# Kernel optimization log

Measured on AMD Instinct MI355X. Metric: run time of the kernel, lower is better.

Reference implementation:

```python
import jax, jax.numpy as jnp
import numpy as np

N, D_IN, D_OUT = 4096, 1024, 1024

def setup_inputs() -> dict:
    key = jax.random.key(0)
    k1, k2, k3, k4 = jax.random.split(key, 4)
    x = jax.random.normal(k1, (N, D_IN), dtype=jnp.float32)
    # original uses torch.rand (uniform [0,1)) for params
    w_query = jax.random.uniform(k2, (D_IN, D_OUT), dtype=jnp.float32)
    w_key = jax.random.uniform(k3, (D_IN, D_OUT), dtype=jnp.float32)
    w_value = jax.random.uniform(k4, (D_IN, D_OUT), dtype=jnp.float32)
    return {"x": x, "w_query": w_query, "w_key": w_key, "w_value": w_value}

def reference(x, w_query, w_key, w_value):
    queries = x @ w_query          # [N, d_out]
    keys = x @ w_key               # [N, d_out]
    values = x @ w_value           # [N, d_out]
    scale = keys.shape[-1] ** 0.5
    scores = queries @ keys.T      # [N, N]
    attn = jax.nn.softmax(scores / scale, axis=-1)
    return attn @ values           # [N, d_out]
```

## Files before the change

kernel.cpp:

```cpp
#include <hip/hip_runtime.h>
#include <math.h>

#define NROWS 4096
#define DDIM  1024

typedef __attribute__((ext_vector_type(8))) short short8;
typedef __attribute__((ext_vector_type(4))) float f32x4;

__device__ __forceinline__ ushort f2bf(float v) {
  union { float f; uint32_t u; } c; c.f = v;
  uint32_t u = c.u;
  uint32_t lsb = (u >> 16) & 1u;
  u += 0x7fffu + lsb;
  return (ushort)(u >> 16);
}
__device__ __forceinline__ float bf2f(ushort h) {
  union { uint32_t u; float f; } c; c.u = ((uint32_t)h) << 16;
  return c.f;
}

__device__ __forceinline__ size_t pidx(int r, int c, int ldt) {
  return ((size_t)((r >> 4) * ldt + (c >> 5))) * 512 +
         ((c >> 3) & 3) * 128 + (r & 15) * 8 + (c & 7);
}
__device__ __forceinline__ size_t pidxs(int r, int c, int ldt) {
  return ((size_t)((r >> 4) * ldt + (c >> 5))) * 1024 +
         ((c >> 3) & 3) * 128 + (r & 15) * 8 + (c & 7);
}

__global__ __launch_bounds__(256) void prep(const float* __restrict__ x,
                                            const float* __restrict__ wq,
                                            const float* __restrict__ wk,
                                            const float* __restrict__ wv,
                                            ushort* Xc,
                                            ushort* Wqc, ushort* Wkc, ushort* Wvh) {
  __shared__ float tl[32][33];
  const int b = blockIdx.x, t = threadIdx.x;
  if (b < 1024) {
    const float4* src = (const float4*)x;
#pragma unroll
    for (int r = 0; r < 4; ++r) {
      int i = b * 1024 + r * 256 + t;
      int row = i >> 8;
      int c = (i & 255) << 2;
      float4 v = src[i];
      ushort4 h, l;
      h.x = f2bf(v.x); l.x = f2bf(v.x - bf2f(h.x));
      h.y = f2bf(v.y); l.y = f2bf(v.y - bf2f(h.y));
      h.z = f2bf(v.z); l.z = f2bf(v.z - bf2f(h.z));
      h.w = f2bf(v.w); l.w = f2bf(v.w - bf2f(h.w));
      size_t o = pidxs(row, c, DDIM / 32);
      *(ushort4*)(Xc + o) = h;
      *(ushort4*)(Xc + o + 512) = l;
    }
  } else {
    const int z = (b - 1024) >> 10;
    const int tile = (b - 1024) & 1023;
    const float* src = z == 0 ? wq : (z == 1 ? wk : wv);
    const int r0 = (tile >> 5) * 32;
    const int c0 = (tile & 31) * 32;
    const int tx = t & 31, ty = t >> 5;
    for (int i = ty; i < 32; i += 8)
      tl[i][tx] = src[(size_t)(r0 + i) * DDIM + c0 + tx];
    __syncthreads();
    if (z == 2) {
      for (int i = ty; i < 32; i += 8) {
        float v = tl[tx][i];
        Wvh[pidx(c0 + i, r0 + tx, DDIM / 32)] = f2bf(v);
      }
    } else {
      ushort* d = z == 0 ? Wqc : Wkc;
      for (int i = ty; i < 32; i += 8) {
        float v = tl[tx][i];
        ushort h = f2bf(v);
        size_t o = pidxs(c0 + i, r0 + tx, DDIM / 32);
        d[o] = h;
        d[o + 512] = f2bf(v - bf2f(h));
      }
    }
  }
}

template <int MI, bool SPLIT, int KT, int SA, int SB>
__device__ __forceinline__ void direct_gemm(const ushort* __restrict__ A,
                                            const ushort* __restrict__ B,
                                            int m0, int n0, f32x4 (*acc)[4]) {
  const int t = threadIdx.x;
  const int wv = t >> 6, ln = t & 63;
  const int arb = (wv >> 1) * (MI * 16), crb = (wv & 1) * 64;
  const int ra = (m0 + arb) >> 4;
  const int rb = (n0 + crb) >> 4;

  uint oA[MI], oB[4];
#pragma unroll
  for (int i = 0; i < MI; ++i) oA[i] = (uint)(ra + i) * (uint)(KT * SA) + (uint)ln * 8u;
#pragma unroll
  for (int j = 0; j < 4; ++j) oB[j] = (uint)(rb + j) * (uint)(KT * SB) + (uint)ln * 8u;

  short8 ah0[MI], al0[MI], bh0[4], bl0[4];
  short8 ah1[MI], al1[MI], bh1[4], bl1[4];

#define DG_LOAD(sidx, AH, AL, BH, BL)                                        \
  {                                                                          \
    uint sa_ = (uint)(sidx) * (uint)SA;                                      \
    uint sb_ = (uint)(sidx) * (uint)SB;                                      \
    _Pragma("unroll") for (int i_ = 0; i_ < MI; ++i_) {                      \
      const ushort* pa_ = A + oA[i_] + sa_;                                  \
      AH[i_] = *(const short8*)pa_;                                          \
      if constexpr (SPLIT) AL[i_] = *(const short8*)(pa_ + 512);             \
    }                                                                        \
    _Pragma("unroll") for (int j_ = 0; j_ < 4; ++j_) {                       \
      const ushort* pb_ = B + oB[j_] + sb_;                                  \
      BH[j_] = *(const short8*)pb_;                                          \
      if constexpr (SPLIT) BL[j_] = *(const short8*)(pb_ + 512);             \
    }                                                                        \
  }

#define DG_MFMA(AH, AL, BH, BL)                                              \
  {                                                                          \
    __builtin_amdgcn_s_setprio(1);                                           \
    _Pragma("unroll") for (int j_ = 0; j_ < 4; ++j_) {                       \
      _Pragma("unroll") for (int i_ = 0; i_ < MI; ++i_) {                    \
        acc[i_][j_] = __builtin_amdgcn_mfma_f32_16x16x32_bf16(               \
            AH[i_], BH[j_], acc[i_][j_], 0, 0, 0);                           \
        if constexpr (SPLIT) {                                               \
          acc[i_][j_] = __builtin_amdgcn_mfma_f32_16x16x32_bf16(             \
              AH[i_], BL[j_], acc[i_][j_], 0, 0, 0);                         \
          acc[i_][j_] = __builtin_amdgcn_mfma_f32_16x16x32_bf16(             \
              AL[i_], BH[j_], acc[i_][j_], 0, 0, 0);                         \
        }                                                                    \
      }                                                                      \
    }                                                                        \
    __builtin_amdgcn_s_setprio(0);                                           \
  }

  DG_LOAD(0, ah0, al0, bh0, bl0);
#pragma unroll 1
  for (int s = 0; s < KT - 2; s += 2) {
    DG_LOAD(s + 1, ah1, al1, bh1, bl1);
    DG_MFMA(ah0, al0, bh0, bl0);
    DG_LOAD(s + 2, ah0, al0, bh0, bl0);
    DG_MFMA(ah1, al1, bh1, bl1);
  }
  DG_LOAD(KT - 1, ah1, al1, bh1, bl1);
  DG_MFMA(ah0, al0, bh0, bl0);
  DG_MFMA(ah1, al1, bh1, bl1);

#undef DG_LOAD
#undef DG_MFMA
}

__global__ __launch_bounds__(256) void gemm_qkv(const ushort* __restrict__ Xc,
                                                const ushort* __restrict__ Wqc,
                                                const ushort* __restrict__ Wkc,
                                                const ushort* __restrict__ Wvh,
                                                ushort* Qc, ushort* Kc, ushort* Vt) {
  const int id = blockIdx.y * 24 + blockIdx.x;
  const int wg = (id & 7) * 96 + (id >> 3);
  const int bx = wg % 24, by = wg / 24;
  const int which = bx % 3;
  const int g = bx / 3;
  const int t = threadIdx.x;
  const int wv = t >> 6, ln = t & 63;
  const int quad = ln >> 4, l16 = ln & 15;

  f32x4 acc[4][4];
#pragma unroll
  for (int i = 0; i < 4; ++i)
#pragma unroll
    for (int j = 0; j < 4; ++j) acc[i][j] = (f32x4){0.f, 0.f, 0.f, 0.f};

  if (which == 2) {
    const int m0 = g * 128;
    const int n0 = by * 128;
    direct_gemm<4, false, DDIM / 32, 512, 1024>(Wvh, Xc, m0, n0, acc);
#pragma unroll
    for (int i = 0; i < 4; ++i)
#pragma unroll
      for (int j = 0; j < 4; ++j) {
        int kv = n0 + (wv & 1) * 64 + j * 16 + l16;
        int d = m0 + (wv >> 1) * 64 + i * 16 + quad * 4;
#pragma unroll
        for (int r2 = 0; r2 < 4; ++r2)
          Vt[pidx(d + r2, kv, NROWS / 32)] = f2bf(acc[i][j][r2]);
      }
  } else {
    const int n0 = g * 128;
    const int m0 = by * 128;
    const ushort* Bc = which ? Wkc : Wqc;
    direct_gemm<4, true, DDIM / 32, 1024, 1024>(Xc, Bc, m0, n0, acc);
    const float scale = which ? 1.0f : 0.03125f;
    ushort* D = which ? Kc : Qc;
#pragma unroll
    for (int i = 0; i < 4; ++i)
#pragma unroll
      for (int j = 0; j < 4; ++j) {
        int col = n0 + (wv & 1) * 64 + j * 16 + l16;
        int rw = m0 + (wv >> 1) * 64 + i * 16 + quad * 4;
#pragma unroll
        for (int r2 = 0; r2 < 4; ++r2) {
          float v = acc[i][j][r2] * scale;
          ushort h = f2bf(v);
          size_t o = pidxs(rw + r2, col, DDIM / 32);
          D[o] = h;
          D[o + 512] = f2bf(v - bf2f(h));
        }
      }
  }
}

__global__ __launch_bounds__(256) void gemm_s(const ushort* __restrict__ Qc,
                                              const ushort* __restrict__ Kc,
                                              float* __restrict__ S) {
  const int bid = blockIdx.y * 32 + blockIdx.x;
  const int xcd = bid & 7, local = bid >> 3;
  const int band = xcd >> 1, half = xcd & 1;
  const int row_l = local & 7, col_l = local >> 3;
  const int m0 = (band * 8 + row_l) * 128;
  const int n0 = (half * 16 + col_l) * 128;
  const int t = threadIdx.x;
  const int wv = t >> 6, ln = t & 63;
  const int quad = ln >> 4, l16 = ln & 15;

  f32x4 acc[4][4];
#pragma unroll
  for (int i = 0; i < 4; ++i)
#pragma unroll
    for (int j = 0; j < 4; ++j) acc[i][j] = (f32x4){0.f, 0.f, 0.f, 0.f};

  direct_gemm<4, true, DDIM / 32, 1024, 1024>(Qc, Kc, m0, n0, acc);

#pragma unroll
  for (int i = 0; i < 4; ++i)
#pragma unroll
    for (int j = 0; j < 4; ++j) {
      int col = n0 + (wv & 1) * 64 + j * 16 + l16;
      int rw = m0 + (wv >> 1) * 64 + i * 16 + quad * 4;
#pragma unroll
      for (int r2 = 0; r2 < 4; ++r2)
        S[(size_t)(rw + r2) * NROWS + col] = acc[i][j][r2];
    }
}

__global__ __launch_bounds__(256) void softmax_pack(const float* __restrict__ S,
                                                    ushort* __restrict__ P) {
  const int row = blockIdx.x, t = threadIdx.x;
  const float* Sr = S + (size_t)row * NROWS;
  const float4* S4 = (const float4*)Sr;
  float4 v[4];
  float mx = -3.4e38f;
#pragma unroll
  for (int c = 0; c < 4; ++c) {
    v[c] = S4[c * 256 + t];
    mx = fmaxf(mx, fmaxf(fmaxf(v[c].x, v[c].y), fmaxf(v[c].z, v[c].w)));
  }
  __shared__ float red[4];
  for (int o = 32; o >= 1; o >>= 1) mx = fmaxf(mx, __shfl_xor(mx, o));
  int wv = t >> 6, ln = t & 63;
  if (ln == 0) red[wv] = mx;
  __syncthreads();
  mx = fmaxf(fmaxf(red[0], red[1]), fmaxf(red[2], red[3]));
  float s = 0.f;
#pragma unroll
  for (int c = 0; c < 4; ++c) {
    v[c].x = __expf(v[c].x - mx);
    v[c].y = __expf(v[c].y - mx);
    v[c].z = __expf(v[c].z - mx);
    v[c].w = __expf(v[c].w - mx);
    s += v[c].x + v[c].y + v[c].z + v[c].w;
  }
  for (int o = 32; o >= 1; o >>= 1) s += __shfl_xor(s, o);
  __syncthreads();
  if (ln == 0) red[wv] = s;
  __syncthreads();
  s = red[0] + red[1] + red[2] + red[3];
  float inv = 1.f / s;
#pragma unroll
  for (int c = 0; c < 4; ++c) {
    ushort4 h;
    h.x = f2bf(v[c].x * inv);
    h.y = f2bf(v[c].y * inv);
    h.z = f2bf(v[c].z * inv);
    h.w = f2bf(v[c].w * inv);
    int c0 = 1024 * c + 4 * t;
    *(ushort4*)(P + pidx(row, c0, NROWS / 32)) = h;
  }
}

__global__ __launch_bounds__(256) void gemm_pv(const ushort* __restrict__ P,
                                               const ushort* __restrict__ Vt,
                                               float* __restrict__ Out) {
  const int n0 = blockIdx.x * 128, m0 = blockIdx.y * 128;
  const int t = threadIdx.x;
  const int wv = t >> 6, ln = t & 63;
  const int quad = ln >> 4, l16 = ln & 15;

  f32x4 acc[4][4];
#pragma unroll
  for (int i = 0; i < 4; ++i)
#pragma unroll
    for (int j = 0; j < 4; ++j) acc[i][j] = (f32x4){0.f, 0.f, 0.f, 0.f};

  direct_gemm<4, false, NROWS / 32, 512, 512>(P, Vt, m0, n0, acc);

#pragma unroll
  for (int i = 0; i < 4; ++i)
#pragma unroll
    for (int j = 0; j < 4; ++j) {
      int col = n0 + (wv & 1) * 64 + j * 16 + l16;
      int rw = m0 + (wv >> 1) * 64 + i * 16 + quad * 4;
#pragma unroll
      for (int r2 = 0; r2 < 4; ++r2)
        Out[(size_t)(rw + r2) * DDIM + col] = acc[i][j][r2];
    }
}

extern "C" void kernel_launch(void* const* d_in, const int* in_sizes, int n_in,
                              void* d_out, int out_size, void* d_ws, size_t ws_size,
                              hipStream_t stream) {
  const float* x  = (const float*)d_in[0];
  const float* wq = (const float*)d_in[1];
  const float* wk = (const float*)d_in[2];
  const float* wv = (const float*)d_in[3];
  char* ws = (char*)d_ws;
  const size_t MB = 1u << 20;

  ushort* Vt  = (ushort*)(ws + 0);
  ushort* Qc  = (ushort*)(ws + 8 * MB);
  ushort* Kc  = (ushort*)(ws + 24 * MB);
  ushort* Pp  = (ushort*)(ws + 8 * MB);
  ushort* Xc  = (ushort*)(ws + 40 * MB);
  ushort* Wqc = (ushort*)(ws + 56 * MB);
  ushort* Wkc = (ushort*)(ws + 60 * MB);
  ushort* Wvh = (ushort*)(ws + 64 * MB);
  float*  S   = (float*)(ws + 40 * MB);
  float*  Out = (float*)d_out;

  prep<<<4096, 256, 0, stream>>>(x, wq, wk, wv, Xc, Wqc, Wkc, Wvh);
  gemm_qkv<<<dim3(24, 32), 256, 0, stream>>>(Xc, Wqc, Wkc, Wvh, Qc, Kc, Vt);
  gemm_s<<<dim3(32, 32), 256, 0, stream>>>(Qc, Kc, S);
  softmax_pack<<<NROWS, 256, 0, stream>>>(S, Pp);
  gemm_pv<<<dim3(8, 32), 256, 0, stream>>>(Pp, Vt, Out);
}
```

Baseline: 321.9 us.

## Rewrite score GEMM with 256x256 tiles and double-buffered LDS async loads

The Q·K^T score kernel moves from a direct-from-global 128x128 tile per 256-thread block to a 256x256 tile per 512-thread block. It stages Q and K panels into a double-buffered 128 KB LDS region using global_load_lds, prefetching the next k-step while MFMAs run on the current one, with priority bumps around the MFMA bursts. The goal is more data reuse per block and hiding global memory latency behind compute. The cost is heavy LDS use and a 128-register accumulator array, which lowers occupancy, plus many barriers per k-step. The prep kernel also switches to nontemporal loads, and the softmax kernel changes vector types.

Result: faster. 315.4 us (-2.0%).

```diff
diff --git a/kernel.cpp b/kernel.cpp
--- a/kernel.cpp
+++ b/kernel.cpp
@@ -17,6 +17,11 @@
 __device__ __forceinline__ float bf2f(ushort h) {
   union { uint32_t u; float f; } c; c.u = ((uint32_t)h) << 16;
   return c.f;
+}
+
+__device__ __forceinline__ void gll16(const void* g, void* l) {
+  __builtin_amdgcn_global_load_lds((const __attribute__((address_space(1))) void*)g,
+                                   (__attribute__((address_space(3))) void*)l, 16, 0, 0);
 }
 
 __device__ __forceinline__ size_t pidx(int r, int c, int ldt) {
@@ -37,13 +42,13 @@
   __shared__ float tl[32][33];
   const int b = blockIdx.x, t = threadIdx.x;
   if (b < 1024) {
-    const float4* src = (const float4*)x;
+    const f32x4* src = (const f32x4*)x;
 #pragma unroll
     for (int r = 0; r < 4; ++r) {
       int i = b * 1024 + r * 256 + t;
       int row = i >> 8;
       int c = (i & 255) << 2;
-      float4 v = src[i];
+      f32x4 v = __builtin_nontemporal_load(src + i);
       ushort4 h, l;
       h.x = f2bf(v.x); l.x = f2bf(v.x - bf2f(h.x));
       h.y = f2bf(v.y); l.y = f2bf(v.y - bf2f(h.y));
@@ -61,7 +66,7 @@
     const int c0 = (tile & 31) * 32;
     const int tx = t & 31, ty = t >> 5;
     for (int i = ty; i < 32; i += 8)
-      tl[i][tx] = src[(size_t)(r0 + i) * DDIM + c0 + tx];
+      tl[i][tx] = __builtin_nontemporal_load(&src[(size_t)(r0 + i) * DDIM + c0 + tx]);
     __syncthreads();
     if (z == 2) {
       for (int i = ty; i < 32; i += 8) {
@@ -209,33 +214,118 @@
   }
 }
 
-__global__ __launch_bounds__(256) void gemm_s(const ushort* __restrict__ Qc,
+__global__ __launch_bounds__(512) void gemm_s(const ushort* __restrict__ Qc,
                                               const ushort* __restrict__ Kc,
                                               float* __restrict__ S) {
-  const int bid = blockIdx.y * 32 + blockIdx.x;
+  __shared__ char smem[2][65536];
+  const int bid = blockIdx.y * 16 + blockIdx.x;
   const int xcd = bid & 7, local = bid >> 3;
-  const int band = xcd >> 1, half = xcd & 1;
-  const int row_l = local & 7, col_l = local >> 3;
-  const int m0 = (band * 8 + row_l) * 128;
-  const int n0 = (half * 16 + col_l) * 128;
+  const int m0 = ((xcd >> 1) * 4 + (local & 3)) * 256;
+  const int n0 = ((xcd & 1) * 8 + (local >> 2)) * 256;
   const int t = threadIdx.x;
-  const int wv = t >> 6, ln = t & 63;
+  const int w = t >> 6, ln = t & 63;
+  const int wr = w >> 2, wc = w & 3;
   const int quad = ln >> 4, l16 = ln & 15;
 
-  f32x4 acc[4][4];
-#pragma unroll
-  for (int i = 0; i < 4; ++i)
+  const char* srcBase = (w < 4)
+      ? (const char*)Qc + (size_t)((m0 >> 4) + w * 4) * 65536
+      : (const char*)Kc + (size_t)((n0 >> 4) + (w - 4) * 4) * 65536;
+  srcBase += ln * 16;
+  char* ldsBase = (char*)smem + w * 8192 + ln * 16;
+
+  f32x4 acc[8][4];
+#pragma unroll
+  for (int i = 0; i < 8; ++i)
 #pragma unroll
     for (int j = 0; j < 4; ++j) acc[i][j] = (f32x4){0.f, 0.f, 0.f, 0.f};
 
-  direct_gemm<4, true, DDIM / 32, 1024, 1024>(Qc, Kc, m0, n0, acc);
-
-#pragma unroll
-  for (int i = 0; i < 4; ++i)
+#pragma unroll
+  for (int u = 0; u < 8; ++u)
+    gll16(srcBase + (u >> 1) * 65536 + (u & 1) * 1024, ldsBase + u * 1024);
+  asm volatile("s_waitcnt vmcnt(0)" ::: "memory");
+  __builtin_amdgcn_s_barrier();
+
+  const char* aB = (char*)smem + (wr * 8) * 2048 + ln * 16;
+  const char* bB = (char*)smem + 32768 + (wc * 4) * 2048 + ln * 16;
+
+#define S_MFMA_PAIR(I, AH0, AL0, AH1, AL1)                                    \
+  {                                                                           \
+    __builtin_amdgcn_s_setprio(1);                                            \
+    _Pragma("unroll") for (int j_ = 0; j_ < 4; ++j_) {                        \
+      acc[I][j_] = __builtin_amdgcn_mfma_f32_16x16x32_bf16(AH0, bh[j_], acc[I][j_], 0, 0, 0);       \
+      acc[I][j_] = __builtin_amdgcn_mfma_f32_16x16x32_bf16(AH0, bl[j_], acc[I][j_], 0, 0, 0);       \
+      acc[I][j_] = __builtin_amdgcn_mfma_f32_16x16x32_bf16(AL0, bh[j_], acc[I][j_], 0, 0, 0);       \
+      acc[I + 1][j_] = __builtin_amdgcn_mfma_f32_16x16x32_bf16(AH1, bh[j_], acc[I + 1][j_], 0, 0, 0); \
+      acc[I + 1][j_] = __builtin_amdgcn_mfma_f32_16x16x32_bf16(AH1, bl[j_], acc[I + 1][j_], 0, 0, 0); \
+      acc[I + 1][j_] = __builtin_amdgcn_mfma_f32_16x16x32_bf16(AL1, bh[j_], acc[I + 1][j_], 0, 0, 0); \
+    }                                                                         \
+    __builtin_amdgcn_s_setprio(0);                                            \
+  }
+
+#pragma unroll 1
+  for (int kt = 0; kt < 32; ++kt) {
+    const int cb = (kt & 1) << 16;
+    const int nb = ((kt + 1) & 1) << 16;
+    const char* srcK = srcBase + (size_t)(kt + 1) * 2048;
+
+    short8 bh[4], bl[4], ah0, al0, ah1, al1;
+
 #pragma unroll
     for (int j = 0; j < 4; ++j) {
-      int col = n0 + (wv & 1) * 64 + j * 16 + l16;
-      int rw = m0 + (wv >> 1) * 64 + i * 16 + quad * 4;
+      bh[j] = *(const short8*)(bB + cb + j * 2048);
+      bl[j] = *(const short8*)(bB + cb + j * 2048 + 1024);
+    }
+    ah0 = *(const short8*)(aB + cb + 0 * 2048);
+    al0 = *(const short8*)(aB + cb + 0 * 2048 + 1024);
+    ah1 = *(const short8*)(aB + cb + 1 * 2048);
+    al1 = *(const short8*)(aB + cb + 1 * 2048 + 1024);
+    if (kt < 31) {
+#pragma unroll
+      for (int u = 0; u < 4; ++u)
+        gll16(srcK + (u >> 1) * 65536 + (u & 1) * 1024, ldsBase + nb + u * 1024);
+    }
+    __builtin_amdgcn_s_barrier();
+    S_MFMA_PAIR(0, ah0, al0, ah1, al1);
+    __builtin_amdgcn_s_barrier();
+
+    ah0 = *(const short8*)(aB + cb + 2 * 2048);
+    al0 = *(const short8*)(aB + cb + 2 * 2048 + 1024);
+    ah1 = *(const short8*)(aB + cb + 3 * 2048);
+    al1 = *(const short8*)(aB + cb + 3 * 2048 + 1024);
+    if (kt < 31) {
+#pragma unroll
+      for (int u = 4; u < 8; ++u)
+        gll16(srcK + (u >> 1) * 65536 + (u & 1) * 1024, ldsBase + nb + u * 1024);
+    }
+    __builtin_amdgcn_s_barrier();
+    S_MFMA_PAIR(2, ah0, al0, ah1, al1);
+    __builtin_amdgcn_s_barrier();
+
+    ah0 = *(const short8*)(aB + cb + 4 * 2048);
+    al0 = *(const short8*)(aB + cb + 4 * 2048 + 1024);
+    ah1 = *(const short8*)(aB + cb + 5 * 2048);
+    al1 = *(const short8*)(aB + cb + 5 * 2048 + 1024);
+    __builtin_amdgcn_s_barrier();
+    S_MFMA_PAIR(4, ah0, al0, ah1, al1);
+    __builtin_amdgcn_s_barrier();
+
+    ah0 = *(const short8*)(aB + cb + 6 * 2048);
+    al0 = *(const short8*)(aB + cb + 6 * 2048 + 1024);
+    ah1 = *(const short8*)(aB + cb + 7 * 2048);
+    al1 = *(const short8*)(aB + cb + 7 * 2048 + 1024);
+    __builtin_amdgcn_s_barrier();
+    S_MFMA_PAIR(6, ah0, al0, ah1, al1);
+    asm volatile("s_waitcnt vmcnt(0)" ::: "memory");
+    __builtin_amdgcn_s_barrier();
+  }
+#undef S_MFMA_PAIR
+
+#pragma unroll
+  for (int i = 0; i < 8; ++i)
+#pragma unroll
+    for (int j = 0; j < 4; ++j) {
+      int col = n0 + wc * 64 + j * 16 + l16;
+      int rw = m0 + wr * 128 + i * 16 + quad * 4;
 #pragma unroll
       for (int r2 = 0; r2 < 4; ++r2)
         S[(size_t)(rw + r2) * NROWS + col] = acc[i][j][r2];
@@ -246,8 +336,8 @@
                                                     ushort* __restrict__ P) {
   const int row = blockIdx.x, t = threadIdx.x;
   const float* Sr = S + (size_t)row * NROWS;
-  const float4* S4 = (const float4*)Sr;
-  float4 v[4];
+  const f32x4* S4 = (const f32x4*)Sr;
+  f32x4 v[4];
   float mx = -3.4e38f;
 #pragma unroll
   for (int c = 0; c < 4; ++c) {
@@ -338,7 +428,7 @@
 
   prep<<<4096, 256, 0, stream>>>(x, wq, wk, wv, Xc, Wqc, Wkc, Wvh);
   gemm_qkv<<<dim3(24, 32), 256, 0, stream>>>(Xc, Wqc, Wkc, Wvh, Qc, Kc, Vt);
-  gemm_s<<<dim3(32, 32), 256, 0, stream>>>(Qc, Kc, S);
+  gemm_s<<<dim3(16, 16), 512, 0, stream>>>(Qc, Kc, S);
   softmax_pack<<<NROWS, 256, 0, stream>>>(S, Pp);
   gemm_pv<<<dim3(8, 32), 256, 0, stream>>>(Pp, Vt, Out);
 }
```
